# Optimization experiments

Measured on AMD Instinct MI355X. Metric: run time of the kernel, lower is better.

The kernel has to match this reference:

```python
import jax, jax.numpy as jnp
import numpy as np

N_NODES = 100000
N_EDGES = 1600000
IN_CH = 64
HEADS = 8
OUT_CH = 16
NEG_SLOPE = 0.2  # PyG GATConv default


def setup_inputs() -> dict:
    key = jax.random.key(0)
    ks = jax.random.split(key, 6)
    x = jax.random.normal(ks[0], (N_NODES, IN_CH), dtype=jnp.float32)
    edge_index = jax.random.randint(ks[1], (2, N_EDGES), 0, N_NODES, dtype=jnp.int32)
    # learned parameters (PyG GATConv: shared lin for src/dst, att vectors, bias for concat output)
    W = jax.random.normal(ks[2], (HEADS * OUT_CH, IN_CH), dtype=jnp.float32) / np.sqrt(IN_CH)
    att_src = jax.random.normal(ks[3], (HEADS, OUT_CH), dtype=jnp.float32) / np.sqrt(OUT_CH)
    att_dst = jax.random.normal(ks[4], (HEADS, OUT_CH), dtype=jnp.float32) / np.sqrt(OUT_CH)
    bias = jax.random.normal(ks[5], (HEADS * OUT_CH,), dtype=jnp.float32) * 0.01
    return {"x": x, "edge_index": edge_index, "W": W,
            "att_src": att_src, "att_dst": att_dst, "bias": bias}


def reference(x, edge_index, W, att_src, att_dst, bias):
    n = x.shape[0]
    # linear projection -> [N, H, C]
    h = (x @ W.T).reshape(n, HEADS, OUT_CH)
    # per-node halves of the attention logit
    a_src = jnp.einsum('nhc,hc->nh', h, att_src)  # [N, H]
    a_dst = jnp.einsum('nhc,hc->nh', h, att_dst)  # [N, H]
    # add self loops (PyG default add_self_loops=True)
    loops = jnp.arange(n, dtype=edge_index.dtype)
    src = jnp.concatenate([edge_index[0], loops])
    dst = jnp.concatenate([edge_index[1], loops])
    # edge attention: leaky_relu then segment-softmax over incoming edges of dst
    e = jax.nn.leaky_relu(a_src[src] + a_dst[dst], NEG_SLOPE)  # [E+N, H]
    e_max = jax.ops.segment_max(e, dst, num_segments=n)
    e = jnp.exp(e - e_max[dst])
    denom = jax.ops.segment_sum(e, dst, num_segments=n)
    alpha = e / (denom[dst] + 1e-16)  # [E+N, H]
    # weighted scatter-add aggregation
    msg = h[src] * alpha[:, :, None]  # [E+N, H, C]
    out = jax.ops.segment_sum(msg, dst, num_segments=n).reshape(n, HEADS * OUT_CH)
    out = out + bias
    # unlinear: act='relu', norm=None
    return jax.nn.relu(out)
```

## Files before the change

kernel.cpp:

```cpp
#include <hip/hip_runtime.h>

#define N_NODESC 100000
#define N_EDGESC 1600000
#define HCC 128
#define E_TOTC (N_EDGESC + N_NODESC)
#define SCAN_NB 391
#define PROJ_NB 782
#define POS_NB 6641
#define WU_NB 36

#define FLAG_AGG 0x40000000u
#define FLAG_PRE 0x80000000u
#define VAL_MASK 0x3fffffffu

__device__ __forceinline__ float lrelu(float v) { return fmaxf(v, 0.2f * v); }
__device__ __forceinline__ unsigned short f2bf(float f) {
    unsigned u = __float_as_uint(f);
    unsigned r = ((u >> 16) & 1u) + 0x7fffu;
    return (unsigned short)((u + r) >> 16);
}

__global__ void wu_pos_kernel(const float* __restrict__ W,
                              const float* __restrict__ att_src, const float* __restrict__ att_dst,
                              float* __restrict__ WT, float* __restrict__ us_g,
                              const int* __restrict__ ei, int* __restrict__ deg,
                              int* __restrict__ posb) {
    if (blockIdx.x < WU_NB) {
        int t = blockIdx.x * 256 + threadIdx.x;
        if (t < 8192) {
            int k = t >> 7, c = t & 127;
            WT[t] = W[c * 64 + k];
        } else if (t < 9216) {
            int o = t - 8192;
            int k = o >> 4, c = o & 15;
            const int h = (c < 8) ? c : c - 8;
            const float* av = (c < 8) ? att_src : att_dst;
            float s = 0.f;
#pragma unroll
            for (int j = 0; j < 16; ++j) s += av[h * 16 + j] * W[(h * 16 + j) * 64 + k];
            us_g[o] = s;
        }
        return;
    }
    int e = (blockIdx.x - WU_NB) * 256 + threadIdx.x;
    if (e >= E_TOTC) return;
    int d = (e < N_EDGESC) ? ei[N_EDGESC + e] : (e - N_EDGESC);
    posb[e] = atomicAdd(&deg[d], 1);
}

__launch_bounds__(256, 2)
__global__ void proj_kernel(const float* __restrict__ x, const float* __restrict__ WT,
                            const float* __restrict__ us_g,
                            unsigned short* __restrict__ h16,
                            float* __restrict__ a_src, float* __restrict__ a_dst) {
    __shared__ float xs[128][68];
    __shared__ float ws[64][132];
    __shared__ float us[64][16];
    const int t = threadIdx.x;
    const int row0 = blockIdx.x * 128;

    const float4* wt4 = (const float4*)WT;
#pragma unroll
    for (int j = 0; j < 8; ++j) {
        int q = t + 256 * j;
        int k = q >> 5, c4 = q & 31;
        *(float4*)&ws[k][c4 * 4] = wt4[q];
    }
    ((float4*)&us[0][0])[t] = ((const float4*)us_g)[t];

#pragma unroll
    for (int j = 0; j < 8; ++j) {
        int f = (t + 256 * j) * 4;
        int r = f >> 6, k = f & 63;
        int gr = row0 + r;
        if (gr >= N_NODESC) gr = N_NODESC - 1;
        float4 v = *(const float4*)&x[(size_t)gr * 64 + k];
        *(float4*)&xs[r][k] = v;
    }
    __syncthreads();

    const int rg = t & 15;
    const int cg = t >> 4;
    float acc[8][8], acca[8];
#pragma unroll
    for (int i = 0; i < 8; ++i) {
        acca[i] = 0.f;
#pragma unroll
        for (int j = 0; j < 8; ++j) acc[i][j] = 0.f;
    }

#pragma unroll 4
    for (int k = 0; k < 64; ++k) {
        float xv[8];
#pragma unroll
        for (int i = 0; i < 8; ++i) xv[i] = xs[rg + 16 * i][k];
        float4 w0 = *(const float4*)&ws[k][4 * cg];
        float4 w1 = *(const float4*)&ws[k][64 + 4 * cg];
        float uv = us[k][cg];
#pragma unroll
        for (int i = 0; i < 8; ++i) {
            acc[i][0] += xv[i] * w0.x; acc[i][1] += xv[i] * w0.y;
            acc[i][2] += xv[i] * w0.z; acc[i][3] += xv[i] * w0.w;
            acc[i][4] += xv[i] * w1.x; acc[i][5] += xv[i] * w1.y;
            acc[i][6] += xv[i] * w1.z; acc[i][7] += xv[i] * w1.w;
            acca[i]   += xv[i] * uv;
        }
    }

#pragma unroll
    for (int i = 0; i < 8; ++i) {
        int gr = row0 + rg + 16 * i;
        if (gr < N_NODESC) {
            ushort4 p0, p1;
            p0.x = f2bf(acc[i][0]); p0.y = f2bf(acc[i][1]); p0.z = f2bf(acc[i][2]); p0.w = f2bf(acc[i][3]);
            p1.x = f2bf(acc[i][4]); p1.y = f2bf(acc[i][5]); p1.z = f2bf(acc[i][6]); p1.w = f2bf(acc[i][7]);
            *(ushort4*)&h16[(size_t)gr * HCC + 4 * cg] = p0;
            *(ushort4*)&h16[(size_t)gr * HCC + 64 + 4 * cg] = p1;
            if (cg < 8) a_src[(size_t)gr * 8 + cg] = acca[i];
            else        a_dst[(size_t)gr * 8 + cg - 8] = acca[i];
        }
    }
}

__global__ void scan_kernel(const int* __restrict__ deg, unsigned* __restrict__ state,
                            int* __restrict__ rowptr) {
    __shared__ int lds[256];
    __shared__ int s_prefix;
    const int b = blockIdx.x, t = threadIdx.x;
    const int i = b * 256 + t;
    const int v = (i < N_NODESC) ? deg[i] : 0;
    lds[t] = v;
    __syncthreads();
    for (int off = 1; off < 256; off <<= 1) {
        int u = 0;
        if (t >= off) u = lds[t - off];
        __syncthreads();
        if (t >= off) lds[t] += u;
        __syncthreads();
    }
    const int incl = lds[t];
    const int total = lds[255];
    if (t == 0) {
        if (b == 0) {
            atomicExch(&state[0], FLAG_PRE | (unsigned)total);
            s_prefix = 0;
        } else {
            atomicExch(&state[b], FLAG_AGG | (unsigned)total);
            unsigned run = 0;
            int j = b - 1;
            while (true) {
                unsigned s = atomicAdd(&state[j], 0u);
                if (s & FLAG_PRE) { run += s & VAL_MASK; break; }
                if (s & FLAG_AGG) { run += s & VAL_MASK; --j; }
            }
            atomicExch(&state[b], FLAG_PRE | ((unsigned)total + run));
            s_prefix = (int)run;
        }
    }
    __syncthreads();
    const int excl = s_prefix + incl - v;
    if (i <= N_NODESC) rowptr[i] = excl;
}

__global__ void scatter_kernel(const int* __restrict__ ei, const int* __restrict__ rowptr,
                               const int* __restrict__ posb, int* __restrict__ colsrc) {
    int e = blockIdx.x * 256 + threadIdx.x;
    if (e >= E_TOTC) return;
    int s, d;
    if (e < N_EDGESC) { s = ei[e]; d = ei[N_EDGESC + e]; }
    else              { s = d = e - N_EDGESC; }
    colsrc[rowptr[d] + posb[e]] = s;
}

__launch_bounds__(256, 8)
__global__ void agg_csr_kernel(const int* __restrict__ rowptr, const int* __restrict__ colsrc,
                               const float* __restrict__ a_src, const float* __restrict__ a_dst,
                               const unsigned* __restrict__ h32,
                               const float* __restrict__ bias, float* __restrict__ out) {
    const int t = threadIdx.x;
    const int L = t & 63;
    const int n = blockIdx.x * 4 + (t >> 6);
    const int hd = L >> 3;
    const int eL = L & 7;

    const int beg = rowptr[n], end = rowptr[n + 1];
    const float ad = a_dst[n * 8 + hd];

    float den = 0.f;
    float acc[16];
#pragma unroll
    for (int j = 0; j < 16; ++j) acc[j] = 0.f;

    int p = beg + eL;
    bool v0 = p < end;
    bool v1 = p + 8 < end;
    int sA = v0 ? colsrc[p] : 0;
    int sB = v1 ? colsrc[p + 8] : 0;
    float avA = v0 ? a_src[sA * 8 + hd] : 0.f;

    while (v0) {
        const uint4* hp = (const uint4*)(h32 + (size_t)sA * 64 + hd * 8);
        const uint4 ha = hp[0];
        const uint4 hb = hp[1];
        const bool v2 = p + 16 < end;
        const int sC = v2 ? colsrc[p + 16] : 0;
        const float avB = v1 ? a_src[sB * 8 + hd] : 0.f;

        const float pr = __expf(lrelu(avA + ad));
        den += pr;
        acc[0]  = fmaf(pr, __uint_as_float(ha.x << 16),         acc[0]);
        acc[1]  = fmaf(pr, __uint_as_float(ha.x & 0xffff0000u), acc[1]);
        acc[2]  = fmaf(pr, __uint_as_float(ha.y << 16),         acc[2]);
        acc[3]  = fmaf(pr, __uint_as_float(ha.y & 0xffff0000u), acc[3]);
        acc[4]  = fmaf(pr, __uint_as_float(ha.z << 16),         acc[4]);
        acc[5]  = fmaf(pr, __uint_as_float(ha.z & 0xffff0000u), acc[5]);
        acc[6]  = fmaf(pr, __uint_as_float(ha.w << 16),         acc[6]);
        acc[7]  = fmaf(pr, __uint_as_float(ha.w & 0xffff0000u), acc[7]);
        acc[8]  = fmaf(pr, __uint_as_float(hb.x << 16),         acc[8]);
        acc[9]  = fmaf(pr, __uint_as_float(hb.x & 0xffff0000u), acc[9]);
        acc[10] = fmaf(pr, __uint_as_float(hb.y << 16),         acc[10]);
        acc[11] = fmaf(pr, __uint_as_float(hb.y & 0xffff0000u), acc[11]);
        acc[12] = fmaf(pr, __uint_as_float(hb.z << 16),         acc[12]);
        acc[13] = fmaf(pr, __uint_as_float(hb.z & 0xffff0000u), acc[13]);
        acc[14] = fmaf(pr, __uint_as_float(hb.w << 16),         acc[14]);
        acc[15] = fmaf(pr, __uint_as_float(hb.w & 0xffff0000u), acc[15]);

        p += 8;
        sA = sB; sB = sC; avA = avB;
        v0 = v1; v1 = v2;
    }

    den += __shfl_xor(den, 1); den += __shfl_xor(den, 2); den += __shfl_xor(den, 4);
#pragma unroll
    for (int j = 0; j < 16; ++j) {
        acc[j] += __shfl_xor(acc[j], 1);
        acc[j] += __shfl_xor(acc[j], 2);
        acc[j] += __shfl_xor(acc[j], 4);
    }
    const float inv = 1.f / (den + 1e-16f);
    float ox = acc[0], oy = acc[1];
#pragma unroll
    for (int j = 1; j < 8; ++j) {
        ox = (eL == j) ? acc[2 * j]     : ox;
        oy = (eL == j) ? acc[2 * j + 1] : oy;
    }
    const float2 b = ((const float2*)bias)[L];
    float2 o;
    o.x = fmaxf(ox * inv + b.x, 0.f);
    o.y = fmaxf(oy * inv + b.y, 0.f);
    ((float2*)out)[(size_t)n * 64 + L] = o;
}

extern "C" void kernel_launch(void* const* d_in, const int* in_sizes, int n_in,
                              void* d_out, int out_size, void* d_ws, size_t ws_size,
                              hipStream_t stream) {
    const float* x       = (const float*)d_in[0];
    const int*   ei      = (const int*)d_in[1];
    const float* W       = (const float*)d_in[2];
    const float* att_src = (const float*)d_in[3];
    const float* att_dst = (const float*)d_in[4];
    const float* bias    = (const float*)d_in[5];
    float* out = (float*)d_out;

    float* ws    = (float*)d_ws;
    unsigned short* h16 = (unsigned short*)ws;
    float* a_src = ws + 6400000;
    float* a_dst = a_src + 800000;
    float* WT    = a_dst + 800000;
    float* us_g  = WT + 8192;
    int* deg     = (int*)(us_g + 1024);
    unsigned* state = (unsigned*)(deg + 100000);
    int* rowptr  = (int*)(state + 392);
    int* posb    = rowptr + 100001;
    int* colsrc  = posb + 1700000;

    hipMemsetAsync(deg, 0, (100000 + 392) * sizeof(int), stream);

    wu_pos_kernel<<<WU_NB + POS_NB, 256, 0, stream>>>(W, att_src, att_dst, WT, us_g,
                                                      ei, deg, posb);
    proj_kernel<<<PROJ_NB, 256, 0, stream>>>(x, WT, us_g, h16, a_src, a_dst);
    scan_kernel<<<SCAN_NB, 256, 0, stream>>>(deg, state, rowptr);
    scatter_kernel<<<(E_TOTC + 255) / 256, 256, 0, stream>>>(ei, rowptr, posb, colsrc);
    agg_csr_kernel<<<N_NODESC / 4, 256, 0, stream>>>(rowptr, colsrc, a_src, a_dst,
                                                     (const unsigned*)h16, bias, out);
}
```

Baseline: 234.9 us.

## Vectorize edge kernels, fold weight prep into projection, unroll aggregation by two

The edge-position and scatter kernels now each handle four edges per thread with int4 loads and stores. The W transpose and attention-vector folding move out of the first kernel and into the projection kernel, which computes them per block in shared memory after issuing its x loads. The aggregation loop processes two edges per lane per iteration with deeper prefetch to expose more memory-level parallelism. The cost is redundant W and attention work in every projection block and higher register pressure in the aggregation kernel.

```diff
diff --git a/kernel.cpp b/kernel.cpp
--- a/kernel.cpp
+++ b/kernel.cpp
@@ -6,8 +6,7 @@
 #define E_TOTC (N_EDGESC + N_NODESC)
 #define SCAN_NB 391
 #define PROJ_NB 782
-#define POS_NB 6641
-#define WU_NB 36
+#define QUAD_NB 1661
 
 #define FLAG_AGG 0x40000000u
 #define FLAG_PRE 0x80000000u
@@ -20,37 +19,31 @@
     return (unsigned short)((u + r) >> 16);
 }
 
-__global__ void wu_pos_kernel(const float* __restrict__ W,
-                              const float* __restrict__ att_src, const float* __restrict__ att_dst,
-                              float* __restrict__ WT, float* __restrict__ us_g,
-                              const int* __restrict__ ei, int* __restrict__ deg,
-                              int* __restrict__ posb) {
-    if (blockIdx.x < WU_NB) {
-        int t = blockIdx.x * 256 + threadIdx.x;
-        if (t < 8192) {
-            int k = t >> 7, c = t & 127;
-            WT[t] = W[c * 64 + k];
-        } else if (t < 9216) {
-            int o = t - 8192;
-            int k = o >> 4, c = o & 15;
-            const int h = (c < 8) ? c : c - 8;
-            const float* av = (c < 8) ? att_src : att_dst;
-            float s = 0.f;
-#pragma unroll
-            for (int j = 0; j < 16; ++j) s += av[h * 16 + j] * W[(h * 16 + j) * 64 + k];
-            us_g[o] = s;
-        }
-        return;
-    }
-    int e = (blockIdx.x - WU_NB) * 256 + threadIdx.x;
-    if (e >= E_TOTC) return;
-    int d = (e < N_EDGESC) ? ei[N_EDGESC + e] : (e - N_EDGESC);
-    posb[e] = atomicAdd(&deg[d], 1);
+__global__ void pos_kernel(const int* __restrict__ ei, int* __restrict__ deg,
+                           int* __restrict__ posb) {
+    const int q = blockIdx.x * 256 + threadIdx.x;
+    const int e0 = q * 4;
+    if (e0 >= E_TOTC) return;
+    int d[4];
+    if (e0 + 3 < N_EDGESC) {
+        int4 dd = *(const int4*)&ei[N_EDGESC + e0];
+        d[0] = dd.x; d[1] = dd.y; d[2] = dd.z; d[3] = dd.w;
+    } else {
+#pragma unroll
+        for (int j = 0; j < 4; ++j) {
+            int e = e0 + j;
+            d[j] = (e < N_EDGESC) ? ei[N_EDGESC + e] : (e - N_EDGESC);
+        }
+    }
+    int p[4];
+#pragma unroll
+    for (int j = 0; j < 4; ++j) p[j] = atomicAdd(&deg[d[j]], 1);
+    *(int4*)&posb[e0] = make_int4(p[0], p[1], p[2], p[3]);
 }
 
 __launch_bounds__(256, 2)
-__global__ void proj_kernel(const float* __restrict__ x, const float* __restrict__ WT,
-                            const float* __restrict__ us_g,
+__global__ void proj_kernel(const float* __restrict__ x, const float* __restrict__ W,
+                            const float* __restrict__ att_src, const float* __restrict__ att_dst,
                             unsigned short* __restrict__ h16,
                             float* __restrict__ a_src, float* __restrict__ a_dst) {
     __shared__ float xs[128][68];
@@ -59,23 +52,38 @@
     const int t = threadIdx.x;
     const int row0 = blockIdx.x * 128;
 
-    const float4* wt4 = (const float4*)WT;
+    float4 xv4[8];
+#pragma unroll
+    for (int j = 0; j < 8; ++j) {
+        int f = (t + 256 * j) * 4;
+        int gr = row0 + (f >> 6);
+        if (gr >= N_NODESC) gr = N_NODESC - 1;
+        xv4[j] = *(const float4*)&x[(size_t)gr * 64 + (f & 63)];
+    }
+    const float4* W4 = (const float4*)W;
 #pragma unroll
     for (int j = 0; j < 8; ++j) {
         int q = t + 256 * j;
-        int k = q >> 5, c4 = q & 31;
-        *(float4*)&ws[k][c4 * 4] = wt4[q];
-    }
-    ((float4*)&us[0][0])[t] = ((const float4*)us_g)[t];
-
+        float4 v = W4[q];
+        int c = q >> 4, k0 = (q & 15) * 4;
+        ws[k0 + 0][c] = v.x; ws[k0 + 1][c] = v.y;
+        ws[k0 + 2][c] = v.z; ws[k0 + 3][c] = v.w;
+    }
+#pragma unroll
+    for (int j = 0; j < 4; ++j) {
+        int o = t + 256 * j;
+        int k = o >> 4, c = o & 15;
+        const int h = c & 7;
+        const float* av = (c < 8) ? att_src : att_dst;
+        float s = 0.f;
+#pragma unroll
+        for (int jj = 0; jj < 16; ++jj) s += av[h * 16 + jj] * W[(h * 16 + jj) * 64 + k];
+        us[k][c] = s;
+    }
 #pragma unroll
     for (int j = 0; j < 8; ++j) {
         int f = (t + 256 * j) * 4;
-        int r = f >> 6, k = f & 63;
-        int gr = row0 + r;
-        if (gr >= N_NODESC) gr = N_NODESC - 1;
-        float4 v = *(const float4*)&x[(size_t)gr * 64 + k];
-        *(float4*)&xs[r][k] = v;
+        *(float4*)&xs[f >> 6][f & 63] = xv4[j];
     }
     __syncthreads();
 
@@ -164,12 +172,29 @@
 
 __global__ void scatter_kernel(const int* __restrict__ ei, const int* __restrict__ rowptr,
                                const int* __restrict__ posb, int* __restrict__ colsrc) {
-    int e = blockIdx.x * 256 + threadIdx.x;
-    if (e >= E_TOTC) return;
-    int s, d;
-    if (e < N_EDGESC) { s = ei[e]; d = ei[N_EDGESC + e]; }
-    else              { s = d = e - N_EDGESC; }
-    colsrc[rowptr[d] + posb[e]] = s;
+    const int q = blockIdx.x * 256 + threadIdx.x;
+    const int e0 = q * 4;
+    if (e0 >= E_TOTC) return;
+    int4 pp = *(const int4*)&posb[e0];
+    int s[4], d[4], p[4] = { pp.x, pp.y, pp.z, pp.w };
+    if (e0 + 3 < N_EDGESC) {
+        int4 ss = *(const int4*)&ei[e0];
+        int4 dd = *(const int4*)&ei[N_EDGESC + e0];
+        s[0] = ss.x; s[1] = ss.y; s[2] = ss.z; s[3] = ss.w;
+        d[0] = dd.x; d[1] = dd.y; d[2] = dd.z; d[3] = dd.w;
+    } else {
+#pragma unroll
+        for (int j = 0; j < 4; ++j) {
+            int e = e0 + j;
+            if (e < N_EDGESC) { s[j] = ei[e]; d[j] = ei[N_EDGESC + e]; }
+            else              { s[j] = d[j] = e - N_EDGESC; }
+        }
+    }
+    int r[4];
+#pragma unroll
+    for (int j = 0; j < 4; ++j) r[j] = rowptr[d[j]];
+#pragma unroll
+    for (int j = 0; j < 4; ++j) colsrc[r[j] + p[j]] = s[j];
 }
 
 __launch_bounds__(256, 8)
@@ -191,43 +216,70 @@
 #pragma unroll
     for (int j = 0; j < 16; ++j) acc[j] = 0.f;
 
-    int p = beg + eL;
-    bool v0 = p < end;
-    bool v1 = p + 8 < end;
-    int sA = v0 ? colsrc[p] : 0;
-    int sB = v1 ? colsrc[p + 8] : 0;
-    float avA = v0 ? a_src[sA * 8 + hd] : 0.f;
-
-    while (v0) {
-        const uint4* hp = (const uint4*)(h32 + (size_t)sA * 64 + hd * 8);
-        const uint4 ha = hp[0];
-        const uint4 hb = hp[1];
-        const bool v2 = p + 16 < end;
-        const int sC = v2 ? colsrc[p + 16] : 0;
-        const float avB = v1 ? a_src[sB * 8 + hd] : 0.f;
-
-        const float pr = __expf(lrelu(avA + ad));
-        den += pr;
-        acc[0]  = fmaf(pr, __uint_as_float(ha.x << 16),         acc[0]);
-        acc[1]  = fmaf(pr, __uint_as_float(ha.x & 0xffff0000u), acc[1]);
-        acc[2]  = fmaf(pr, __uint_as_float(ha.y << 16),         acc[2]);
-        acc[3]  = fmaf(pr, __uint_as_float(ha.y & 0xffff0000u), acc[3]);
-        acc[4]  = fmaf(pr, __uint_as_float(ha.z << 16),         acc[4]);
-        acc[5]  = fmaf(pr, __uint_as_float(ha.z & 0xffff0000u), acc[5]);
-        acc[6]  = fmaf(pr, __uint_as_float(ha.w << 16),         acc[6]);
-        acc[7]  = fmaf(pr, __uint_as_float(ha.w & 0xffff0000u), acc[7]);
-        acc[8]  = fmaf(pr, __uint_as_float(hb.x << 16),         acc[8]);
-        acc[9]  = fmaf(pr, __uint_as_float(hb.x & 0xffff0000u), acc[9]);
-        acc[10] = fmaf(pr, __uint_as_float(hb.y << 16),         acc[10]);
-        acc[11] = fmaf(pr, __uint_as_float(hb.y & 0xffff0000u), acc[11]);
-        acc[12] = fmaf(pr, __uint_as_float(hb.z << 16),         acc[12]);
-        acc[13] = fmaf(pr, __uint_as_float(hb.z & 0xffff0000u), acc[13]);
-        acc[14] = fmaf(pr, __uint_as_float(hb.w << 16),         acc[14]);
-        acc[15] = fmaf(pr, __uint_as_float(hb.w & 0xffff0000u), acc[15]);
-
-        p += 8;
-        sA = sB; sB = sC; avA = avB;
-        v0 = v1; v1 = v2;
+    int pA = beg + eL;
+    int pB = beg + 8 + eL;
+    bool vA0 = pA < end,       vB0 = pB < end;
+    bool vA1 = pA + 16 < end,  vB1 = pB + 16 < end;
+    int sA0 = vA0 ? colsrc[pA] : 0;
+    int sB0 = vB0 ? colsrc[pB] : 0;
+    int sA1 = vA1 ? colsrc[pA + 16] : 0;
+    int sB1 = vB1 ? colsrc[pB + 16] : 0;
+    float aA0 = vA0 ? a_src[sA0 * 8 + hd] : 0.f;
+    float aB0 = vB0 ? a_src[sB0 * 8 + hd] : 0.f;
+
+    while (vA0) {
+        const uint4* hpA = (const uint4*)(h32 + (size_t)sA0 * 64 + hd * 8);
+        const uint4 ha0 = hpA[0], ha1 = hpA[1];
+        const uint4* hpB = (const uint4*)(h32 + (size_t)sB0 * 64 + hd * 8);
+        const uint4 hb0 = hpB[0], hb1 = hpB[1];
+        const bool vA2 = pA + 32 < end, vB2 = pB + 32 < end;
+        const int sA2 = vA2 ? colsrc[pA + 32] : 0;
+        const int sB2 = vB2 ? colsrc[pB + 32] : 0;
+        const float aA1 = vA1 ? a_src[sA1 * 8 + hd] : 0.f;
+        const float aB1 = vB1 ? a_src[sB1 * 8 + hd] : 0.f;
+
+        const float prA = __expf(lrelu(aA0 + ad));
+        const float prB = vB0 ? __expf(lrelu(aB0 + ad)) : 0.f;
+        den += prA + prB;
+
+        acc[0]  = fmaf(prA, __uint_as_float(ha0.x << 16),         acc[0]);
+        acc[1]  = fmaf(prA, __uint_as_float(ha0.x & 0xffff0000u), acc[1]);
+        acc[2]  = fmaf(prA, __uint_as_float(ha0.y << 16),         acc[2]);
+        acc[3]  = fmaf(prA, __uint_as_float(ha0.y & 0xffff0000u), acc[3]);
+        acc[4]  = fmaf(prA, __uint_as_float(ha0.z << 16),         acc[4]);
+        acc[5]  = fmaf(prA, __uint_as_float(ha0.z & 0xffff0000u), acc[5]);
+        acc[6]  = fmaf(prA, __uint_as_float(ha0.w << 16),         acc[6]);
+        acc[7]  = fmaf(prA, __uint_as_float(ha0.w & 0xffff0000u), acc[7]);
+        acc[8]  = fmaf(prA, __uint_as_float(ha1.x << 16),         acc[8]);
+        acc[9]  = fmaf(prA, __uint_as_float(ha1.x & 0xffff0000u), acc[9]);
+        acc[10] = fmaf(prA, __uint_as_float(ha1.y << 16),         acc[10]);
+        acc[11] = fmaf(prA, __uint_as_float(ha1.y & 0xffff0000u), acc[11]);
+        acc[12] = fmaf(prA, __uint_as_float(ha1.z << 16),         acc[12]);
+        acc[13] = fmaf(prA, __uint_as_float(ha1.z & 0xffff0000u), acc[13]);
+        acc[14] = fmaf(prA, __uint_as_float(ha1.w << 16),         acc[14]);
+        acc[15] = fmaf(prA, __uint_as_float(ha1.w & 0xffff0000u), acc[15]);
+
+        acc[0]  = fmaf(prB, __uint_as_float(hb0.x << 16),         acc[0]);
+        acc[1]  = fmaf(prB, __uint_as_float(hb0.x & 0xffff0000u), acc[1]);
+        acc[2]  = fmaf(prB, __uint_as_float(hb0.y << 16),         acc[2]);
+        acc[3]  = fmaf(prB, __uint_as_float(hb0.y & 0xffff0000u), acc[3]);
+        acc[4]  = fmaf(prB, __uint_as_float(hb0.z << 16),         acc[4]);
+        acc[5]  = fmaf(prB, __uint_as_float(hb0.z & 0xffff0000u), acc[5]);
+        acc[6]  = fmaf(prB, __uint_as_float(hb0.w << 16),         acc[6]);
+        acc[7]  = fmaf(prB, __uint_as_float(hb0.w & 0xffff0000u), acc[7]);
+        acc[8]  = fmaf(prB, __uint_as_float(hb1.x << 16),         acc[8]);
+        acc[9]  = fmaf(prB, __uint_as_float(hb1.x & 0xffff0000u), acc[9]);
+        acc[10] = fmaf(prB, __uint_as_float(hb1.y << 16),         acc[10]);
+        acc[11] = fmaf(prB, __uint_as_float(hb1.y & 0xffff0000u), acc[11]);
+        acc[12] = fmaf(prB, __uint_as_float(hb1.z << 16),         acc[12]);
+        acc[13] = fmaf(prB, __uint_as_float(hb1.z & 0xffff0000u), acc[13]);
+        acc[14] = fmaf(prB, __uint_as_float(hb1.w << 16),         acc[14]);
+        acc[15] = fmaf(prB, __uint_as_float(hb1.w & 0xffff0000u), acc[15]);
+
+        pA += 16; pB += 16;
+        sA0 = sA1; sB0 = sB1; sA1 = sA2; sB1 = sB2;
+        aA0 = aA1; aB0 = aB1;
+        vA0 = vA1; vB0 = vB1; vA1 = vA2; vB1 = vB2;
     }
 
     den += __shfl_xor(den, 1); den += __shfl_xor(den, 2); den += __shfl_xor(den, 4);
@@ -266,9 +318,7 @@
     unsigned short* h16 = (unsigned short*)ws;
     float* a_src = ws + 6400000;
     float* a_dst = a_src + 800000;
-    float* WT    = a_dst + 800000;
-    float* us_g  = WT + 8192;
-    int* deg     = (int*)(us_g + 1024);
+    int* deg     = (int*)(a_dst + 800000);
     unsigned* state = (unsigned*)(deg + 100000);
     int* rowptr  = (int*)(state + 392);
     int* posb    = rowptr + 100001;
@@ -276,11 +326,10 @@
 
     hipMemsetAsync(deg, 0, (100000 + 392) * sizeof(int), stream);
 
-    wu_pos_kernel<<<WU_NB + POS_NB, 256, 0, stream>>>(W, att_src, att_dst, WT, us_g,
-                                                      ei, deg, posb);
-    proj_kernel<<<PROJ_NB, 256, 0, stream>>>(x, WT, us_g, h16, a_src, a_dst);
+    pos_kernel<<<QUAD_NB, 256, 0, stream>>>(ei, deg, posb);
+    proj_kernel<<<PROJ_NB, 256, 0, stream>>>(x, W, att_src, att_dst, h16, a_src, a_dst);
     scan_kernel<<<SCAN_NB, 256, 0, stream>>>(deg, state, rowptr);
-    scatter_kernel<<<(E_TOTC + 255) / 256, 256, 0, stream>>>(ei, rowptr, posb, colsrc);
+    scatter_kernel<<<QUAD_NB, 256, 0, stream>>>(ei, rowptr, posb, colsrc);
     agg_csr_kernel<<<N_NODESC / 4, 256, 0, stream>>>(rowptr, colsrc, a_src, a_dst,
                                                      (const unsigned*)h16, bias, out);
 }
```

Result: slower. 339.7 us (+44.7%).
